# Optimization experiments

Measured on AMD Instinct MI355X. Metric: run time of the kernel, lower is better.

## Reference

```python
import jax, jax.numpy as jnp
import numpy as np

MAX_DISPARITY = 192


def _cost_volume(L, R, D):
    """Banded stereo correlation.

    cost[n, j, h, x] = sum_c L[n,c,h,x] * R[n,c,h,x-j], zero when x < j.
    Equivalent to the original full (W,W) matmul followed by per-disparity
    diagonal extraction + left zero-pad, but computed as D shifted
    dot-products (honors the banded structure).
    """
    N, C, H, W = L.shape
    Rp = jnp.pad(R, ((0, 0), (0, 0), (0, 0), (D - 1, 0)))  # left zero-pad

    def step(_, j):
        Rs = jax.lax.dynamic_slice_in_dim(Rp, D - 1 - j, W, axis=3)  # R shifted right by j
        c = jnp.einsum('nchw,nchw->nhw', L, Rs)
        return None, c

    _, cv = jax.lax.scan(step, None, jnp.arange(D))  # (D, N, H, W)
    return jnp.transpose(cv, (1, 0, 2, 3))  # (N, D, H, W)


def setup_inputs() -> dict:
    key = jax.random.key(0)
    ks = jax.random.split(key, 6)
    shapes = [(1, 32, 256, 512), (1, 32, 128, 256), (1, 32, 64, 128)]
    inp = {}
    for i, s in enumerate(shapes):
        inp[f'left{i}'] = jax.random.normal(ks[2 * i], s, dtype=jnp.float32)
        inp[f'right{i}'] = jax.random.normal(ks[2 * i + 1], s, dtype=jnp.float32)
    return inp


def reference(left0, right0, left1, right1, left2, right2):
    lefts = [left0, left1, left2]
    rights = [right0, right1, right2]
    max_disparity = min(MAX_DISPARITY, lefts[0].shape[-1])
    cost_volumes = []
    for i, (L, R) in enumerate(zip(lefts, rights)):
        D = max_disparity // (2 ** i)
        cost_volumes.append(_cost_volume(L, R, D))
    return tuple(cost_volumes)
```

## Files before the change

### kernel.cpp

```cpp
#include <hip/hip_runtime.h>


#define NBLK_TOTAL 1344
#define SRB 80

typedef float vf4 __attribute__((ext_vector_type(4)));
typedef float f32x4 __attribute__((ext_vector_type(4)));
typedef _Float16 h4 __attribute__((ext_vector_type(4)));
typedef _Float16 h8 __attribute__((ext_vector_type(8)));

template<int DG>
__device__ __forceinline__ void epilogue(const f32x4 (&acc0)[13], const f32x4 (&acc1)[13],
                                         float* __restrict__ Ep, float* __restrict__ o,
                                         int H, int W, int h, int x0,
                                         int t, int lm, int kg, int q0)
{
    #pragma unroll
    for (int jg = 0; jg < DG; ++jg) {
        if (jg == 0) {
            int b0 = (q0)     * 516 + (12 & 1) * 256 + lm * 16 + 4 * kg;
            int b1 = (q0 + 1) * 516 + (12 & 1) * 256 + lm * 16 + 4 * kg;
            *(f32x4*)&Ep[b0] = acc0[12];
            *(f32x4*)&Ep[b1] = acc1[12];
        }
        {
            int b0 = (q0)     * 516 + ((11 - jg) & 1) * 256 + lm * 16 + 4 * kg;
            int b1 = (q0 + 1) * 516 + ((11 - jg) & 1) * 256 + lm * 16 + 4 * kg;
            *(f32x4*)&Ep[b0] = acc0[11 - jg];
            *(f32x4*)&Ep[b1] = acc1[11 - jg];
        }
        __syncthreads();
        const int s12 = jg & 1;
        const int s11 = s12 ^ 1;
        #pragma unroll
        for (int r = 0; r < 2; ++r) {
            int jo = 8 * r + (t >> 5);
            int j  = 16 * jg + jo;
            int xs = 4 * (t & 31);
            int mt = xs >> 4;
            int mb = xs & 15;
            vf4 v;
            #pragma unroll
            for (int i = 0; i < 4; ++i) {
                int m = mb + i;
                int slot = (m >= jo) ? s12 : s11;
                int n = (m - jo) & 15;
                v[i] = Ep[mt * 516 + slot * 256 + n * 16 + m];
            }
            float* p = o + ((size_t)j * H + h) * W + x0 + xs;
            __builtin_nontemporal_store(v, (vf4*)p);
        }
        if (jg + 1 < DG) __syncthreads();
    }
}

__global__ __launch_bounds__(256, 2)
void cost_volume_fused(const float* __restrict__ L0, const float* __restrict__ R0,
                       const float* __restrict__ L1, const float* __restrict__ R1,
                       const float* __restrict__ L2, const float* __restrict__ R2,
                       float* __restrict__ out)
{
    __shared__ __align__(16) char St[448 * SRB];
    __shared__ __align__(16) float Ep[8 * 516];

    const int id = (blockIdx.x & 7) * 168 + (blockIdx.x >> 3);

    const float* L; const float* R; float* o;
    int H, W, D, bx, h;
    if (id < 1024) {
        L = L0; R = R0; o = out;
        H = 256; W = 512; D = 192;
        bx = id & 3; h = id >> 2;
    } else if (id < 1280) {
        int r = id - 1024;
        L = L1; R = R1; o = out + (size_t)192 * 256 * 512;
        H = 128; W = 256; D = 96;
        bx = r & 1; h = r >> 1;
    } else {
        int r = id - 1280;
        L = L2; R = R2; o = out + (size_t)192 * 256 * 512 + (size_t)96 * 128 * 256;
        H = 64; W = 128; D = 48;
        bx = 0; h = r;
    }

    const int x0 = bx * 128;
    const int t  = threadIdx.x;
    const int l  = t & 63;
    const int w_ = t >> 6;

    const size_t HW = (size_t)H * W;
    const float* Lb = L + (size_t)h * W;
    const float* Rb = R + (size_t)h * W;

    char* Sb = (char*)St;

    {
        const int c0 = (t >> 5) * 4;
        const int x4 = t & 31;
        const float* gp = Lb + (size_t)c0 * HW + x0 + 4 * x4;
        vf4 v0 = *(const vf4*)(gp);
        vf4 v1 = *(const vf4*)(gp + HW);
        vf4 v2 = *(const vf4*)(gp + 2 * HW);
        vf4 v3 = *(const vf4*)(gp + 3 * HW);
        const int chk = (((c0 >> 3) ^ (x4 & 3)) << 4) | ((c0 & 7) << 1);
        #pragma unroll
        for (int xi = 0; xi < 4; ++xi) {
            int row = 4 * x4 + xi;
            h4 hv = { (_Float16)v0[xi], (_Float16)v1[xi],
                      (_Float16)v2[xi], (_Float16)v3[xi] };
            *(h4*)(Sb + row * SRB + chk) = hv;
        }
    }
    #pragma unroll
    for (int k = 0; k < 3; ++k) {
        int idm = t + k * 256;
        if (idm < 640) {
            int c0 = (idm / 80) * 4;
            int x4 = idm - (idm / 80) * 80;
            int g = x0 - 192 + 4 * x4;
            vf4 v0 = (vf4)(0.f), v1 = (vf4)(0.f), v2 = (vf4)(0.f), v3 = (vf4)(0.f);
            if (g >= 0) {
                const float* gp = Rb + (size_t)c0 * HW + g;
                v0 = *(const vf4*)(gp);
                v1 = *(const vf4*)(gp + HW);
                v2 = *(const vf4*)(gp + 2 * HW);
                v3 = *(const vf4*)(gp + 3 * HW);
            }
            const int chk = (((c0 >> 3) ^ (x4 & 3)) << 4) | ((c0 & 7) << 1);
            #pragma unroll
            for (int xi = 0; xi < 4; ++xi) {
                int row = 128 + 4 * x4 + xi;
                h4 hv = { (_Float16)v0[xi], (_Float16)v1[xi],
                          (_Float16)v2[xi], (_Float16)v3[xi] };
                *(h4*)(Sb + row * SRB + chk) = hv;
            }
        }
    }
    __syncthreads();

    const int lm = l & 15;
    const int kg = l >> 4;
    const int q0 = 2 * w_;
    const int rsw = (lm >> 2) & 3;

    f32x4 acc0[13], acc1[13];
    #pragma unroll
    for (int i = 0; i < 13; ++i) { acc0[i] = (f32x4)(0.f); acc1[i] = (f32x4)(0.f); }

    const int rowA0 = 16 * q0 + lm;
    const int rowA1 = rowA0 + 16;
    h8 a0 = *(const h8*)(Sb + rowA0 * SRB + ((kg ^ rsw) << 4));
    h8 a1 = *(const h8*)(Sb + rowA1 * SRB + ((kg ^ rsw) << 4));

    #pragma unroll
    for (int nt = 0; nt <= 13; ++nt) {
        int rowB = 128 + 16 * (q0 + nt) + lm;
        h8 b = *(const h8*)(Sb + rowB * SRB + ((kg ^ rsw) << 4));
        if (nt <= 12)
            acc0[nt] = __builtin_amdgcn_mfma_f32_16x16x32_f16(a0, b, acc0[nt], 0, 0, 0);
        if (nt >= 1)
            acc1[nt - 1] = __builtin_amdgcn_mfma_f32_16x16x32_f16(a1, b, acc1[nt - 1], 0, 0, 0);
    }

    if (D == 192)      epilogue<12>(acc0, acc1, Ep, o, H, W, h, x0, t, lm, kg, q0);
    else if (D == 96)  epilogue<6>(acc0, acc1, Ep, o, H, W, h, x0, t, lm, kg, q0);
    else               epilogue<3>(acc0, acc1, Ep, o, H, W, h, x0, t, lm, kg, q0);
}

extern "C" void kernel_launch(void* const* d_in, const int* in_sizes, int n_in,
                              void* d_out, int out_size, void* d_ws, size_t ws_size,
                              hipStream_t stream)
{
    const float* L0 = (const float*)d_in[0];
    const float* R0 = (const float*)d_in[1];
    const float* L1 = (const float*)d_in[2];
    const float* R1 = (const float*)d_in[3];
    const float* L2 = (const float*)d_in[4];
    const float* R2 = (const float*)d_in[5];
    float* out = (float*)d_out;

    cost_volume_fused<<<dim3(NBLK_TOTAL), dim3(256), 0, stream>>>(
        L0, R0, L1, R1, L2, R2, out);
}
```

Before: 166.2 us.

## Make epilogue per-wave with private LDS staging and drop block barriers

Each wave now stages its own accumulator tiles in a private LDS region and writes only its own 32-column slice of the output. The block-wide __syncthreads between diagonal-extraction steps go away, so waves no longer stall on each other during the store-heavy epilogue. The LDS row stride is padded to 17 floats to reduce bank conflicts, and launch bounds are raised to 3 blocks per CU to allow more overlap. Correctness relies on wave-level execution ordering within the private region instead of explicit barriers, and each store row becomes 128 bytes wide instead of 512.

```diff
diff --git a/kernel.cpp b/kernel.cpp
--- a/kernel.cpp
+++ b/kernel.cpp
@@ -3,6 +3,8 @@
 
 #define NBLK_TOTAL 1344
 #define SRB 80
+#define EPT 272
+#define EPW 1088
 
 typedef float vf4 __attribute__((ext_vector_type(4)));
 typedef float f32x4 __attribute__((ext_vector_type(4)));
@@ -10,58 +12,56 @@
 typedef _Float16 h8 __attribute__((ext_vector_type(8)));
 
 template<int DG>
-__device__ __forceinline__ void epilogue(const f32x4 (&acc0)[13], const f32x4 (&acc1)[13],
-                                         float* __restrict__ Ep, float* __restrict__ o,
-                                         int H, int W, int h, int x0,
-                                         int t, int lm, int kg, int q0)
+__device__ __forceinline__ void epilogue_w(const f32x4 (&acc0)[13], const f32x4 (&acc1)[13],
+                                           float* __restrict__ Ew, float* __restrict__ o,
+                                           int H, int W, int h, int xw,
+                                           int l, int lm, int kg)
 {
+    const int jo0 = l >> 3;
+    const int xbl = (l & 7) * 4;
+    const int mt  = xbl >> 4;
+    const int mb  = xbl & 15;
+    const int dep = lm * 17 + 4 * kg;
+
     #pragma unroll
     for (int jg = 0; jg < DG; ++jg) {
         if (jg == 0) {
-            int b0 = (q0)     * 516 + (12 & 1) * 256 + lm * 16 + 4 * kg;
-            int b1 = (q0 + 1) * 516 + (12 & 1) * 256 + lm * 16 + 4 * kg;
-            *(f32x4*)&Ep[b0] = acc0[12];
-            *(f32x4*)&Ep[b1] = acc1[12];
+            *(f32x4*)&Ew[(0 * 2 + 0) * EPT + dep] = acc0[12];
+            *(f32x4*)&Ew[(1 * 2 + 0) * EPT + dep] = acc1[12];
         }
         {
-            int b0 = (q0)     * 516 + ((11 - jg) & 1) * 256 + lm * 16 + 4 * kg;
-            int b1 = (q0 + 1) * 516 + ((11 - jg) & 1) * 256 + lm * 16 + 4 * kg;
-            *(f32x4*)&Ep[b0] = acc0[11 - jg];
-            *(f32x4*)&Ep[b1] = acc1[11 - jg];
+            const int slot = (11 - jg) & 1;
+            *(f32x4*)&Ew[(0 * 2 + slot) * EPT + dep] = acc0[11 - jg];
+            *(f32x4*)&Ew[(1 * 2 + slot) * EPT + dep] = acc1[11 - jg];
         }
-        __syncthreads();
         const int s12 = jg & 1;
         const int s11 = s12 ^ 1;
         #pragma unroll
         for (int r = 0; r < 2; ++r) {
-            int jo = 8 * r + (t >> 5);
+            int jo = 8 * r + jo0;
             int j  = 16 * jg + jo;
-            int xs = 4 * (t & 31);
-            int mt = xs >> 4;
-            int mb = xs & 15;
             vf4 v;
             #pragma unroll
             for (int i = 0; i < 4; ++i) {
                 int m = mb + i;
                 int slot = (m >= jo) ? s12 : s11;
                 int n = (m - jo) & 15;
-                v[i] = Ep[mt * 516 + slot * 256 + n * 16 + m];
+                v[i] = Ew[(mt * 2 + slot) * EPT + n * 17 + m];
             }
-            float* p = o + ((size_t)j * H + h) * W + x0 + xs;
+            float* p = o + ((size_t)j * H + h) * W + xw + xbl;
             __builtin_nontemporal_store(v, (vf4*)p);
         }
-        if (jg + 1 < DG) __syncthreads();
     }
 }
 
-__global__ __launch_bounds__(256, 2)
+__global__ __launch_bounds__(256, 3)
 void cost_volume_fused(const float* __restrict__ L0, const float* __restrict__ R0,
                        const float* __restrict__ L1, const float* __restrict__ R1,
                        const float* __restrict__ L2, const float* __restrict__ R2,
                        float* __restrict__ out)
 {
     __shared__ __align__(16) char St[448 * SRB];
-    __shared__ __align__(16) float Ep[8 * 516];
+    __shared__ __align__(16) float Ep[4 * EPW];
 
     const int id = (blockIdx.x & 7) * 168 + (blockIdx.x >> 3);
 
@@ -162,9 +162,11 @@
             acc1[nt - 1] = __builtin_amdgcn_mfma_f32_16x16x32_f16(a1, b, acc1[nt - 1], 0, 0, 0);
     }
 
-    if (D == 192)      epilogue<12>(acc0, acc1, Ep, o, H, W, h, x0, t, lm, kg, q0);
-    else if (D == 96)  epilogue<6>(acc0, acc1, Ep, o, H, W, h, x0, t, lm, kg, q0);
-    else               epilogue<3>(acc0, acc1, Ep, o, H, W, h, x0, t, lm, kg, q0);
+    float* Ew = Ep + w_ * EPW;
+    const int xw = x0 + 32 * w_;
+    if (D == 192)      epilogue_w<12>(acc0, acc1, Ew, o, H, W, h, xw, l, lm, kg);
+    else if (D == 96)  epilogue_w<6>(acc0, acc1, Ew, o, H, W, h, xw, l, lm, kg);
+    else               epilogue_w<3>(acc0, acc1, Ew, o, H, W, h, xw, l, lm, kg);
 }
 
 extern "C" void kernel_launch(void* const* d_in, const int* in_sizes, int n_in,
```

Measured after the change: 167.5 us. About the same (+0.8%).
